# Optimization experiments

Measured on AMD Instinct MI355X. Metric: run time of the kernel, lower is better.

## Reference

```python
import jax, jax.numpy as jnp
import numpy as np

B, M, FIN, FOUT, K, E = 4, 50000, 128, 128, 4, 800000


def setup_inputs() -> dict:
    key = jax.random.key(0)
    ks = jax.random.split(key, 8)
    x = jax.random.normal(ks[0], (B, M, FIN), dtype=jnp.float32)
    L_rows = jax.random.randint(ks[1], (E,), 0, M, dtype=jnp.int32)
    L_cols = jax.random.randint(ks[2], (E,), 0, M, dtype=jnp.int32)
    # stands in for the rescaled (0.75 * (2L/lmax - I)) Laplacian values
    L_vals = jax.random.normal(ks[3], (E,), dtype=jnp.float32) * 0.05
    stddev = 1.0 / np.sqrt(FIN * (K + 0.5) / 2.0)
    kernel = jax.random.normal(ks[4], (K * FIN, FOUT), dtype=jnp.float32) * stddev
    W_down = jax.random.normal(ks[5], (FOUT, FOUT // 8), dtype=jnp.float32) * (1.0 / np.sqrt(FOUT))
    b_down = jnp.zeros((FOUT // 8,), dtype=jnp.float32)
    W_up = jax.random.normal(ks[6], (FOUT // 8, FOUT), dtype=jnp.float32) * (1.0 / np.sqrt(FOUT // 8))
    b_up = jnp.zeros((FOUT,), dtype=jnp.float32)
    return {"x": x, "L_vals": L_vals, "L_rows": L_rows, "L_cols": L_cols,
            "kernel": kernel, "W_down": W_down, "b_down": b_down,
            "W_up": W_up, "b_up": b_up}


def reference(x, L_vals, L_rows, L_cols, kernel, W_down, b_down, W_up, b_up):
    B_, M_, Fin = x.shape
    K_ = kernel.shape[0] // Fin

    def spmm(X):  # sparse L [M,M] @ dense X [M, D]
        return jax.ops.segment_sum(L_vals[:, None] * X[L_cols], L_rows, num_segments=M_)

    # Chebyshev recurrence, operating on [M, Fin*B] like the TF code
    x0 = x.transpose(1, 2, 0).reshape(M_, Fin * B_)
    stack = [x0]
    if K_ > 1:
        x1 = spmm(x0)
        stack.append(x1)
    for _ in range(2, K_):
        x2 = 2.0 * spmm(x1) - x0
        stack.append(x2)
        x0, x1 = x1, x2

    # [K,M,Fin*B] -> [K,M,Fin,B] -> [B,M,Fin,K] -> [B*M, Fin*K]
    xs = jnp.stack(stack, axis=0).reshape(K_, M_, Fin, B_)
    xs = xs.transpose(3, 1, 2, 0).reshape(B_ * M_, Fin * K_)
    y = (xs @ kernel).reshape(B_, M_, -1)
    y = jax.nn.relu(y)

    # SE block: avg-pool over nodes, down (swish), up (sigmoid), scale
    s = jnp.mean(y, axis=1, keepdims=True)          # [B, 1, Fout]
    d = jax.nn.swish(s @ W_down + b_down)           # [B, 1, Fout/8]
    u = jax.nn.sigmoid(d @ W_up + b_up)             # [B, 1, Fout]
    return y * u
```

## Files before the change

### kernel.cpp

```cpp
#include <hip/hip_runtime.h>
#include <hip/hip_bf16.h>

#define BB 4
#define MM 50000
#define FINF 128
#define FOUTF 128
#define KCH 4
#define EE 800000
#define NROWS (BB*MM)
#define XC 512
#define CD 512
#define SLABS 4
#define SC (XC/SLABS)
#define SCB 512
#define NSB ((MM + SCB - 1)/SCB)
#define GXB ((MM + 255)/256)

__device__ __forceinline__ float bf2f(unsigned short u){
    union{unsigned int i; float f;} v; v.i = ((unsigned int)u) << 16; return v.f;
}
__device__ __forceinline__ unsigned short f2bf(float f){
    union{float f; unsigned int i;} v; v.f = f;
    unsigned int r = v.i + 0x7FFF + ((v.i >> 16) & 1);
    return (unsigned short)(r >> 16);
}

typedef __bf16 bf16x8 __attribute__((ext_vector_type(8)));
typedef float  f32x4  __attribute__((ext_vector_type(4)));

typedef __attribute__((address_space(3))) unsigned int       lds_uint;
typedef const __attribute__((address_space(1))) unsigned int gbl_uint;

__global__ __launch_bounds__(256) void k_init_x0(const float* __restrict__ x,
                                                 unsigned short* __restrict__ X0){
    int tid = blockIdx.x*256 + threadIdx.x;
    if (tid >= BB*MM*FINF/4) return;
    int f4 = tid & 31;
    int t  = tid >> 5;
    int m  = t % MM, b = t / MM;
    float4 v = ((const float4*)x)[tid];
    ushort4 o;
    o.x = f2bf(v.x); o.y = f2bf(v.y); o.z = f2bf(v.z); o.w = f2bf(v.w);
    *(ushort4*)(X0 + (size_t)m*XC + b*FINF + f4*4) = o;
}

__global__ __launch_bounds__(256) void k_prepw(const float* __restrict__ kern,
                                               unsigned short* __restrict__ Wt){
    int tid = blockIdx.x*256 + threadIdx.x;
    int c = tid & 511, n = tid >> 9;
    int kc = c >> 7, f = c & 127;
    int ns = n >> 4, l16 = n & 15;
    int ks = c >> 5, rem = c & 31, g = rem >> 3, j = rem & 7;
    int lane = g*16 + l16;
    Wt[((ns*16 + ks)*64 + lane)*8 + j] = f2bf(kern[(f*KCH + kc)*FOUTF + n]);
}

__global__ __launch_bounds__(256) void k_hist(const int* __restrict__ rows, int* __restrict__ counts){
    int e = blockIdx.x*256 + threadIdx.x;
    if (e < EE) atomicAdd(&counts[rows[e]], 1);
}

__global__ __launch_bounds__(256) void k_scanA(const int* __restrict__ counts, int* __restrict__ part){
    __shared__ int red[256];
    int b = blockIdx.x, t = threadIdx.x;
    int i = b*SCB + t;
    int s = 0;
    if (i < MM) s += counts[i];
    if (i + 256 < (b+1)*SCB && i + 256 < MM) s += counts[i+256];
    red[t] = s; __syncthreads();
    for (int d = 128; d > 0; d >>= 1){
        if (t < d) red[t] += red[t+d];
        __syncthreads();
    }
    if (t == 0) part[b] = red[0];
}

__global__ __launch_bounds__(128) void k_scanB(int* __restrict__ part){
    __shared__ int sh[128];
    int t = threadIdx.x;
    sh[t] = (t < NSB) ? part[t] : 0;
    __syncthreads();
    for (int d = 1; d < 128; d <<= 1){
        int v = (t >= d) ? sh[t-d] : 0;
        __syncthreads();
        sh[t] += v;
        __syncthreads();
    }
    if (t < NSB) part[t] = sh[t];
}

__global__ __launch_bounds__(256) void k_scanC(const int* __restrict__ counts, const int* __restrict__ part,
                                               int* __restrict__ offs, int* __restrict__ cursor){
    __shared__ int sh[256];
    int b = blockIdx.x, t = threadIdx.x;
    int base = (b == 0) ? 0 : part[b-1];
    int i0 = b*SCB + 2*t;
    int c0 = (i0     < MM) ? counts[i0]   : 0;
    int c1 = (i0 + 1 < MM) ? counts[i0+1] : 0;
    sh[t] = c0 + c1; __syncthreads();
    for (int d = 1; d < 256; d <<= 1){
        int v = (t >= d) ? sh[t-d] : 0;
        __syncthreads();
        sh[t] += v;
        __syncthreads();
    }
    int excl = base + sh[t] - (c0 + c1);
    if (i0 < MM){ offs[i0] = excl;      cursor[i0] = excl; }
    if (i0 + 1 < MM){ offs[i0+1] = excl + c0; cursor[i0+1] = excl + c0; }
    if (b == gridDim.x-1 && t == 255) offs[MM] = EE;
}

__global__ __launch_bounds__(256) void k_scatter(const int* __restrict__ rows, const int* __restrict__ cols,
                                                 const float* __restrict__ vals, int* __restrict__ cursor,
                                                 int2* __restrict__ edges){
    int e = blockIdx.x*256 + threadIdx.x;
    if (e >= EE) return;
    int r = rows[e];
    int pos = atomicAdd(&cursor[r], 1);
    edges[pos] = make_int2(cols[e], __float_as_int(vals[e]));
}

__global__ __launch_bounds__(256) void k_spmm_slab(const unsigned short* __restrict__ Xin,
                                                   const unsigned short* __restrict__ Xprev,
                                                   unsigned short* __restrict__ Xout,
                                                   const int* __restrict__ offs,
                                                   const int2* __restrict__ edges,
                                                   float alpha, int sub, int cbase){
    int m    = blockIdx.x*4 + (threadIdx.x >> 6);
    int lane = threadIdx.x & 63;
    size_t c0 = (size_t)cbase + lane*2;
    int start = offs[m], end = offs[m+1];
    float a0 = 0.f, a1 = 0.f;

    int nb = (end - start) & ~3;
    int burst_end = start + nb;
    int j = start;

    int2 ee[4];
    if (j < burst_end){
        #pragma unroll
        for (int q = 0; q < 4; ++q) ee[q] = edges[j+q];
    }
    while (j < burst_end){
        int2 e_[4];
        #pragma unroll
        for (int q = 0; q < 4; ++q) e_[q] = ee[q];
        j += 4;
        if (j < burst_end){
            #pragma unroll
            for (int q = 0; q < 4; ++q) ee[q] = edges[j+q];
        }
        ushort2 xv[4];
        #pragma unroll
        for (int q = 0; q < 4; ++q)
            xv[q] = *(const ushort2*)(Xin + (size_t)e_[q].x*XC + c0);
        #pragma unroll
        for (int q = 0; q < 4; ++q){
            float val = __int_as_float(e_[q].y);
            a0 += val*bf2f(xv[q].x); a1 += val*bf2f(xv[q].y);
        }
    }
    for (; j < end; ++j){
        int2 e = edges[j];
        float val = __int_as_float(e.y);
        ushort2 xv = *(const ushort2*)(Xin + (size_t)e.x*XC + c0);
        a0 += val*bf2f(xv.x); a1 += val*bf2f(xv.y);
    }

    a0 *= alpha; a1 *= alpha;
    if (sub){
        ushort2 pv = *(const ushort2*)(Xprev + (size_t)m*XC + c0);
        a0 -= bf2f(pv.x); a1 -= bf2f(pv.y);
    }
    ushort2 o; o.x = f2bf(a0); o.y = f2bf(a1);
    *(ushort2*)(Xout + (size_t)m*XC + c0) = o;
}

__global__ __launch_bounds__(256, 2) void k_gemm(const unsigned short* __restrict__ X0,
                                                 const unsigned short* __restrict__ X1,
                                                 const unsigned short* __restrict__ X2,
                                                 const unsigned short* __restrict__ X3,
                                                 const unsigned short* __restrict__ Wt,
                                                 float* __restrict__ Y,
                                                 float* __restrict__ Ypart){
    const int wave = threadIdx.x >> 6;
    const int lane = threadIdx.x & 63;
    const int l16  = lane & 15;
    const int g    = lane >> 4;
    const int bidx = blockIdx.y;
    const int m0   = blockIdx.x*256;

    __shared__ unsigned short As[2][8192];
    __shared__ unsigned short Bs[2][4096];

    const unsigned short* const Xs[4] = {X0, X1, X2, X3};

    f32x4 acc[4][8];
    #pragma unroll
    for (int i = 0; i < 4; ++i)
        #pragma unroll
        for (int j = 0; j < 8; ++j) acc[i][j] = (f32x4){0.f,0.f,0.f,0.f};

    auto stage = [&](int buf, int ks){
        const unsigned short* Xb = Xs[ks >> 2];
        const int f0 = (ks & 3)*64;
        #pragma unroll
        for (int q = 0; q < 4; ++q){
            int row = q*64 + wave*16 + (lane >> 2);
            int mr  = m0 + row; if (mr >= MM) mr = MM-1;
            int inner = ((lane & 3)*16) ^ ((row & 6) << 3);
            const char* src = (const char*)Xb + (size_t)mr*1024 + bidx*256 + f0 + inner;
            lds_uint* dst = (lds_uint*)(&As[buf][(q*4096 + wave*1024)/2]);
            __builtin_amdgcn_global_load_lds((gbl_uint*)src, dst, 16, 0, 0);
        }
        #pragma unroll
        for (int q = 0; q < 2; ++q){
            int ns = q*4 + wave;
            const char* src = (const char*)Wt + (size_t)(ns*16 + ks)*1024 + lane*16;
            lds_uint* dst = (lds_uint*)(&Bs[buf][ns*512]);
            __builtin_amdgcn_global_load_lds((gbl_uint*)src, dst, 16, 0, 0);
        }
    };

    stage(0, 0);
    __syncthreads();

    for (int ks = 0; ks < 16; ++ks){
        const int buf = ks & 1;
        if (ks < 15) stage(buf ^ 1, ks + 1);

        bf16x8 a[4];
        #pragma unroll
        for (int i = 0; i < 4; ++i){
            int rr = wave*64 + i*16 + l16;
            int phys = rr*64 + ((g*16) ^ ((rr & 6) << 3));
            a[i] = *(const bf16x8*)((const char*)&As[buf][0] + phys);
        }
        #pragma unroll
        for (int ns = 0; ns < 8; ++ns){
            bf16x8 b = *(const bf16x8*)(&Bs[buf][ns*512 + lane*8]);
            #pragma unroll
            for (int i = 0; i < 4; ++i)
                acc[i][ns] = __builtin_amdgcn_mfma_f32_16x16x32_bf16(a[i], b, acc[i][ns], 0, 0, 0);
        }
        __syncthreads();
    }

    __shared__ float ldsum[4][FOUTF];
    float csum[8];
    #pragma unroll
    for (int ns = 0; ns < 8; ++ns) csum[ns] = 0.f;

    #pragma unroll
    for (int i = 0; i < 4; ++i){
        #pragma unroll
        for (int reg = 0; reg < 4; ++reg){
            int mr = m0 + wave*64 + i*16 + g*4 + reg;
            if (mr < MM){
                #pragma unroll
                for (int ns = 0; ns < 8; ++ns){
                    float v = acc[i][ns][reg];
                    v = v > 0.f ? v : 0.f;
                    Y[((size_t)bidx*MM + mr)*FOUTF + ns*16 + l16] = v;
                    csum[ns] += v;
                }
            }
        }
    }
    #pragma unroll
    for (int ns = 0; ns < 8; ++ns){
        float v = csum[ns];
        v += __shfl_xor(v, 16);
        v += __shfl_xor(v, 32);
        csum[ns] = v;
    }
    if (lane < 16){
        #pragma unroll
        for (int ns = 0; ns < 8; ++ns) ldsum[wave][ns*16 + lane] = csum[ns];
    }
    __syncthreads();
    int t = threadIdx.x;
    if (t < FOUTF){
        float s = ldsum[0][t] + ldsum[1][t] + ldsum[2][t] + ldsum[3][t];
        Ypart[((size_t)bidx*GXB + blockIdx.x)*FOUTF + t] = s;
    }
}

__global__ __launch_bounds__(128) void k_se(const float* __restrict__ Ypart,
                                            const float* __restrict__ Wd, const float* __restrict__ bd,
                                            const float* __restrict__ Wu, const float* __restrict__ bu,
                                            float* __restrict__ u){
    int b = blockIdx.x, t = threadIdx.x;
    __shared__ float sm[128];
    __shared__ float dsh[16];
    float s = 0.f;
    for (int j = 0; j < GXB; ++j) s += Ypart[((size_t)b*GXB + j)*FOUTF + t];
    sm[t] = s * (1.0f/MM);
    __syncthreads();
    if (t < 16){
        float a = bd[t];
        for (int f = 0; f < 128; ++f) a += sm[f]*Wd[f*16 + t];
        dsh[t] = a / (1.f + expf(-a));
    }
    __syncthreads();
    float a = bu[t];
    for (int j = 0; j < 16; ++j) a += dsh[j]*Wu[j*FOUTF + t];
    u[b*FOUTF + t] = 1.f/(1.f + expf(-a));
}

__global__ __launch_bounds__(256) void k_scale(const float* __restrict__ Y, const float* __restrict__ u,
                                               float* __restrict__ out){
    int tid = blockIdx.x*256 + threadIdx.x;
    if (tid >= NROWS*FOUTF/4) return;
    int b  = tid / (MM*FOUTF/4);
    int f4 = tid & 31;
    float4 yv = ((const float4*)Y)[tid];
    float4 uv = *(const float4*)(u + b*FOUTF + f4*4);
    float4 o;
    o.x = yv.x*uv.x; o.y = yv.y*uv.y; o.z = yv.z*uv.z; o.w = yv.w*uv.w;
    ((float4*)out)[tid] = o;
}

extern "C" void kernel_launch(void* const* d_in, const int* in_sizes, int n_in,
                              void* d_out, int out_size, void* d_ws, size_t ws_size,
                              hipStream_t stream){
    (void)in_sizes; (void)n_in; (void)out_size; (void)ws_size;
    const float* x    = (const float*)d_in[0];
    const float* lv   = (const float*)d_in[1];
    const int*   lr   = (const int*)d_in[2];
    const int*   lc   = (const int*)d_in[3];
    const float* kern = (const float*)d_in[4];
    const float* Wd   = (const float*)d_in[5];
    const float* bd   = (const float*)d_in[6];
    const float* Wu   = (const float*)d_in[7];
    const float* bu   = (const float*)d_in[8];
    float* out = (float*)d_out;

    char* w = (char*)d_ws;
    size_t off = 0;
    auto take = [&](size_t bytes)->char*{
        char* p = w + off; off += (bytes + 255) & ~(size_t)255; return p;
    };
    unsigned short* X[4];
    for (int i = 0; i < 4; ++i) X[i] = (unsigned short*)take((size_t)MM*XC*2);
    float* Y           = (float*)take((size_t)NROWS*FOUTF*4);
    unsigned short* Wt = (unsigned short*)take((size_t)FOUTF*CD*2);
    int* counts        = (int*)take((size_t)MM*4);
    int* offs          = (int*)take((size_t)(MM+1)*4);
    int* cursor        = (int*)take((size_t)MM*4);
    int2* edges        = (int2*)take((size_t)EE*8);
    int* part          = (int*)take((size_t)NSB*4);
    float* Ypart       = (float*)take((size_t)BB*GXB*FOUTF*4);
    float* u           = (float*)take((size_t)BB*FOUTF*4);

    hipMemsetAsync(counts, 0, MM*4, stream);

    k_init_x0<<<25000, 256, 0, stream>>>(x, X[0]);
    k_prepw<<<256, 256, 0, stream>>>(kern, Wt);
    k_hist<<<(EE+255)/256, 256, 0, stream>>>(lr, counts);
    k_scanA<<<NSB, 256, 0, stream>>>(counts, part);
    k_scanB<<<1, 128, 0, stream>>>(part);
    k_scanC<<<NSB, 256, 0, stream>>>(counts, part, offs, cursor);
    k_scatter<<<(EE+255)/256, 256, 0, stream>>>(lr, lc, lv, cursor, edges);

    for (int s = 0; s < SLABS; ++s){
        int cbase = s*SC;
        k_spmm_slab<<<MM/4, 256, 0, stream>>>(X[0], X[0], X[1], offs, edges, 1.0f, 0, cbase);
        k_spmm_slab<<<MM/4, 256, 0, stream>>>(X[1], X[0], X[2], offs, edges, 2.0f, 1, cbase);
        k_spmm_slab<<<MM/4, 256, 0, stream>>>(X[2], X[1], X[3], offs, edges, 2.0f, 1, cbase);
    }

    dim3 ggemm(GXB, BB);
    k_gemm<<<ggemm, 256, 0, stream>>>(X[0], X[1], X[2], X[3], Wt, Y, Ypart);

    k_se<<<BB, 128, 0, stream>>>(Ypart, Wd, bd, Wu, bu, u);
    k_scale<<<25000, 256, 0, stream>>>(Y, u, out);
}
```

Baseline: 790.9 us.

## Replace slab SpMM with XCD-aware column-strip SpMM splitting edges across lane groups

Replaces the four-slab loop of SpMM launches with a single launch per Chebyshev step. Each block id is decoded so that each of the 8 XCDs handles a fixed 64-column strip (16 strips over two halves), which keeps each XCD's L2 working set to its own columns. Within a wave, four 16-lane groups process different edges in parallel, each lane loading 4 bytes, and the partial sums are reduced with shuffles. Edge column indices are pre-shifted to byte offsets in the scatter kernel to save address arithmetic. The cost is extra shuffle reductions, masked tail loads, and reliance on the hardware assigning consecutive blocks round-robin across XCDs.

```diff
diff --git a/kernel.cpp b/kernel.cpp
--- a/kernel.cpp
+++ b/kernel.cpp
@@ -10,11 +10,12 @@
 #define NROWS (BB*MM)
 #define XC 512
 #define CD 512
-#define SLABS 4
-#define SC (XC/SLABS)
 #define SCB 512
 #define NSB ((MM + SCB - 1)/SCB)
 #define GXB ((MM + 255)/256)
+#define NSS 16
+#define RPB 16
+#define RBS (MM/RPB)
 
 __device__ __forceinline__ float bf2f(unsigned short u){
     union{unsigned int i; float f;} v; v.i = ((unsigned int)u) << 16; return v.f;
@@ -117,63 +118,59 @@
     if (e >= EE) return;
     int r = rows[e];
     int pos = atomicAdd(&cursor[r], 1);
-    edges[pos] = make_int2(cols[e], __float_as_int(vals[e]));
-}
-
-__global__ __launch_bounds__(256) void k_spmm_slab(const unsigned short* __restrict__ Xin,
-                                                   const unsigned short* __restrict__ Xprev,
-                                                   unsigned short* __restrict__ Xout,
-                                                   const int* __restrict__ offs,
-                                                   const int2* __restrict__ edges,
-                                                   float alpha, int sub, int cbase){
-    int m    = blockIdx.x*4 + (threadIdx.x >> 6);
-    int lane = threadIdx.x & 63;
-    size_t c0 = (size_t)cbase + lane*2;
-    int start = offs[m], end = offs[m+1];
+    edges[pos] = make_int2(cols[e] << 10, __float_as_int(vals[e]));
+}
+
+__global__ __launch_bounds__(1024) void k_spmm_x(const unsigned short* __restrict__ Xin,
+                                                 const unsigned short* __restrict__ Xprev,
+                                                 unsigned short* __restrict__ Xout,
+                                                 const int* __restrict__ offs,
+                                                 const int2* __restrict__ edges,
+                                                 float alpha, int sub){
+    const int i    = blockIdx.x;
+    const int xcd  = i & 7;
+    const int j2   = i >> 3;
+    const int half = (j2 >= RBS) ? 1 : 0;
+    const int ss   = xcd + (half << 3);
+    const int rb   = j2 - half*RBS;
+    const int wave = threadIdx.x >> 6;
+    const int m    = rb*RPB + wave;
+    const int lane = threadIdx.x & 63;
+    const int qg   = lane >> 4;
+    const int cl   = lane & 15;
+    const int cb   = ss*64 + cl*4;
+
+    const int start = offs[m], end = offs[m+1];
     float a0 = 0.f, a1 = 0.f;
-
-    int nb = (end - start) & ~3;
-    int burst_end = start + nb;
-    int j = start;
-
-    int2 ee[4];
-    if (j < burst_end){
-        #pragma unroll
-        for (int q = 0; q < 4; ++q) ee[q] = edges[j+q];
-    }
-    while (j < burst_end){
-        int2 e_[4];
-        #pragma unroll
-        for (int q = 0; q < 4; ++q) e_[q] = ee[q];
-        j += 4;
-        if (j < burst_end){
-            #pragma unroll
-            for (int q = 0; q < 4; ++q) ee[q] = edges[j+q];
-        }
-        ushort2 xv[4];
-        #pragma unroll
-        for (int q = 0; q < 4; ++q)
-            xv[q] = *(const ushort2*)(Xin + (size_t)e_[q].x*XC + c0);
-        #pragma unroll
-        for (int q = 0; q < 4; ++q){
-            float val = __int_as_float(e_[q].y);
-            a0 += val*bf2f(xv[q].x); a1 += val*bf2f(xv[q].y);
-        }
-    }
-    for (; j < end; ++j){
-        int2 e = edges[j];
-        float val = __int_as_float(e.y);
-        ushort2 xv = *(const ushort2*)(Xin + (size_t)e.x*XC + c0);
-        a0 += val*bf2f(xv.x); a1 += val*bf2f(xv.y);
-    }
-
+    const char* __restrict__ bp = (const char*)Xin;
+    const long long* __restrict__ ep = (const long long*)edges;
+    for (int j = start; j < end; j += 8){
+        #pragma unroll
+        for (int q = 0; q < 2; ++q){
+            int je = j + q*4 + qg;
+            bool ok = je < end;
+            long long ev = __builtin_nontemporal_load(ep + (ok ? je : 0));
+            float val = ok ? __int_as_float((int)(ev >> 32)) : 0.f;
+            unsigned int xv = *(const unsigned int*)(bp + (unsigned)(int)ev + cb);
+            union{unsigned int u; float f;} lo, hi;
+            lo.u = xv << 16; hi.u = xv & 0xffff0000u;
+            a0 += val*lo.f; a1 += val*hi.f;
+        }
+    }
+    a0 += __shfl_xor(a0, 16); a0 += __shfl_xor(a0, 32);
+    a1 += __shfl_xor(a1, 16); a1 += __shfl_xor(a1, 32);
     a0 *= alpha; a1 *= alpha;
+    size_t ob = (size_t)m*1024 + cb;
     if (sub){
-        ushort2 pv = *(const ushort2*)(Xprev + (size_t)m*XC + c0);
-        a0 -= bf2f(pv.x); a1 -= bf2f(pv.y);
-    }
-    ushort2 o; o.x = f2bf(a0); o.y = f2bf(a1);
-    *(ushort2*)(Xout + (size_t)m*XC + c0) = o;
+        unsigned int pv = *(const unsigned int*)((const char*)Xprev + ob);
+        union{unsigned int u; float f;} lo, hi;
+        lo.u = pv << 16; hi.u = pv & 0xffff0000u;
+        a0 -= lo.f; a1 -= hi.f;
+    }
+    if (qg == 0){
+        unsigned int o = ((unsigned int)f2bf(a1) << 16) | (unsigned int)f2bf(a0);
+        *(unsigned int*)((char*)Xout + ob) = o;
+    }
 }
 
 __global__ __launch_bounds__(256, 2) void k_gemm(const unsigned short* __restrict__ X0,
@@ -363,12 +360,9 @@
     k_scanC<<<NSB, 256, 0, stream>>>(counts, part, offs, cursor);
     k_scatter<<<(EE+255)/256, 256, 0, stream>>>(lr, lc, lv, cursor, edges);
 
-    for (int s = 0; s < SLABS; ++s){
-        int cbase = s*SC;
-        k_spmm_slab<<<MM/4, 256, 0, stream>>>(X[0], X[0], X[1], offs, edges, 1.0f, 0, cbase);
-        k_spmm_slab<<<MM/4, 256, 0, stream>>>(X[1], X[0], X[2], offs, edges, 2.0f, 1, cbase);
-        k_spmm_slab<<<MM/4, 256, 0, stream>>>(X[2], X[1], X[3], offs, edges, 2.0f, 1, cbase);
-    }
+    k_spmm_x<<<NSS*RBS, 1024, 0, stream>>>(X[0], X[0], X[1], offs, edges, 1.0f, 0);
+    k_spmm_x<<<NSS*RBS, 1024, 0, stream>>>(X[1], X[0], X[2], offs, edges, 2.0f, 1);
+    k_spmm_x<<<NSS*RBS, 1024, 0, stream>>>(X[2], X[1], X[3], offs, edges, 2.0f, 1);
 
     dim3 ggemm(GXB, BB);
     k_gemm<<<ggemm, 256, 0, stream>>>(X[0], X[1], X[2], X[3], Wt, Y, Ypart);
```

After: 1.666 ms. +110.6%, slower.

## Replace slabbed SpMM with full-width 16-byte-per-lane SpMM and fuse scan

Applied to the files above, without the earlier changes.

The SpMM is no longer split into four 128-column slabs (12 launches). Each wave now processes a full 512-column bf16 row, with each lane loading 16 bytes per edge and edges walked once per Chebyshev step. Column indices are pre-shifted into byte offsets during scatter, and tail edges are padded by masking instead of a scalar remainder loop. The separate scanB kernel is removed: each scanC block sums the preceding partials itself, which costs a little redundant work and drops one launch. Wider per-lane loads raise register use and give up the L2 locality the slabbing provided for the gathered rows.

```diff
diff --git a/kernel.cpp b/kernel.cpp
--- a/kernel.cpp
+++ b/kernel.cpp
@@ -10,8 +10,6 @@
 #define NROWS (BB*MM)
 #define XC 512
 #define CD 512
-#define SLABS 4
-#define SC (XC/SLABS)
 #define SCB 512
 #define NSB ((MM + SCB - 1)/SCB)
 #define GXB ((MM + 255)/256)
@@ -75,29 +73,18 @@
     if (t == 0) part[b] = red[0];
 }
 
-__global__ __launch_bounds__(128) void k_scanB(int* __restrict__ part){
-    __shared__ int sh[128];
-    int t = threadIdx.x;
-    sh[t] = (t < NSB) ? part[t] : 0;
-    __syncthreads();
-    for (int d = 1; d < 128; d <<= 1){
-        int v = (t >= d) ? sh[t-d] : 0;
-        __syncthreads();
-        sh[t] += v;
-        __syncthreads();
-    }
-    if (t < NSB) part[t] = sh[t];
-}
-
 __global__ __launch_bounds__(256) void k_scanC(const int* __restrict__ counts, const int* __restrict__ part,
                                                int* __restrict__ offs, int* __restrict__ cursor){
     __shared__ int sh[256];
+    __shared__ int pp[NSB];
     int b = blockIdx.x, t = threadIdx.x;
-    int base = (b == 0) ? 0 : part[b-1];
+    if (t < NSB) pp[t] = part[t];
     int i0 = b*SCB + 2*t;
     int c0 = (i0     < MM) ? counts[i0]   : 0;
     int c1 = (i0 + 1 < MM) ? counts[i0+1] : 0;
     sh[t] = c0 + c1; __syncthreads();
+    int base = 0;
+    for (int i = 0; i < b; ++i) base += pp[i];
     for (int d = 1; d < 256; d <<= 1){
         int v = (t >= d) ? sh[t-d] : 0;
         __syncthreads();
@@ -117,63 +104,96 @@
     if (e >= EE) return;
     int r = rows[e];
     int pos = atomicAdd(&cursor[r], 1);
-    edges[pos] = make_int2(cols[e], __float_as_int(vals[e]));
-}
-
-__global__ __launch_bounds__(256) void k_spmm_slab(const unsigned short* __restrict__ Xin,
-                                                   const unsigned short* __restrict__ Xprev,
-                                                   unsigned short* __restrict__ Xout,
-                                                   const int* __restrict__ offs,
-                                                   const int2* __restrict__ edges,
-                                                   float alpha, int sub, int cbase){
-    int m    = blockIdx.x*4 + (threadIdx.x >> 6);
-    int lane = threadIdx.x & 63;
-    size_t c0 = (size_t)cbase + lane*2;
-    int start = offs[m], end = offs[m+1];
-    float a0 = 0.f, a1 = 0.f;
-
-    int nb = (end - start) & ~3;
-    int burst_end = start + nb;
-    int j = start;
-
-    int2 ee[4];
-    if (j < burst_end){
-        #pragma unroll
-        for (int q = 0; q < 4; ++q) ee[q] = edges[j+q];
-    }
-    while (j < burst_end){
-        int2 e_[4];
-        #pragma unroll
-        for (int q = 0; q < 4; ++q) e_[q] = ee[q];
-        j += 4;
-        if (j < burst_end){
-            #pragma unroll
-            for (int q = 0; q < 4; ++q) ee[q] = edges[j+q];
-        }
-        ushort2 xv[4];
-        #pragma unroll
-        for (int q = 0; q < 4; ++q)
-            xv[q] = *(const ushort2*)(Xin + (size_t)e_[q].x*XC + c0);
-        #pragma unroll
-        for (int q = 0; q < 4; ++q){
-            float val = __int_as_float(e_[q].y);
-            a0 += val*bf2f(xv[q].x); a1 += val*bf2f(xv[q].y);
-        }
-    }
-    for (; j < end; ++j){
-        int2 e = edges[j];
-        float val = __int_as_float(e.y);
-        ushort2 xv = *(const ushort2*)(Xin + (size_t)e.x*XC + c0);
-        a0 += val*bf2f(xv.x); a1 += val*bf2f(xv.y);
-    }
-
-    a0 *= alpha; a1 *= alpha;
+    edges[pos] = make_int2(cols[e] << 10, __float_as_int(vals[e]));
+}
+
+__global__ __launch_bounds__(256) void k_spmm_w(const unsigned short* __restrict__ Xin,
+                                                const unsigned short* __restrict__ Xprev,
+                                                unsigned short* __restrict__ Xout,
+                                                const int* __restrict__ offs,
+                                                const int2* __restrict__ edges,
+                                                float alpha, int sub){
+    const int m    = blockIdx.x*4 + (threadIdx.x >> 6);
+    const int lane = threadIdx.x & 63;
+    const int cb   = lane*16;
+    const int start = offs[m], end = offs[m+1];
+
+    float acc[8];
+    #pragma unroll
+    for (int d = 0; d < 8; ++d) acc[d] = 0.f;
+
+    const char* __restrict__ bp = (const char*)Xin;
+    const long long* __restrict__ ep = (const long long*)edges;
+
+    if (start < end){
+        const long long base = ep[start];
+        const int basec = (int)base;
+        int  c[4]; float v[4];
+        {
+            #pragma unroll
+            for (int q = 0; q < 4; ++q){
+                int je = start + q;
+                bool ok = je < end;
+                long long e = ok ? ep[je] : base;
+                c[q] = ok ? (int)e : basec;
+                v[q] = ok ? __int_as_float((int)(e >> 32)) : 0.f;
+            }
+        }
+        int j = start;
+        while (j < end){
+            int cc[4]; float vv[4];
+            #pragma unroll
+            for (int q = 0; q < 4; ++q){ cc[q] = c[q]; vv[q] = v[q]; }
+            j += 4;
+            if (j < end){
+                #pragma unroll
+                for (int q = 0; q < 4; ++q){
+                    int je = j + q;
+                    bool ok = je < end;
+                    long long e = ok ? ep[je] : base;
+                    c[q] = ok ? (int)e : basec;
+                    v[q] = ok ? __int_as_float((int)(e >> 32)) : 0.f;
+                }
+            }
+            uint4 x[4];
+            #pragma unroll
+            for (int q = 0; q < 4; ++q)
+                x[q] = *(const uint4*)(bp + (unsigned)cc[q] + cb);
+            #pragma unroll
+            for (int q = 0; q < 4; ++q){
+                const unsigned int* xw = (const unsigned int*)&x[q];
+                #pragma unroll
+                for (int d = 0; d < 4; ++d){
+                    unsigned int u = xw[d];
+                    union{unsigned int ui; float f;} lo, hi;
+                    lo.ui = u << 16; hi.ui = u & 0xffff0000u;
+                    acc[d*2]   += vv[q]*lo.f;
+                    acc[d*2+1] += vv[q]*hi.f;
+                }
+            }
+        }
+    }
+
+    #pragma unroll
+    for (int d = 0; d < 8; ++d) acc[d] *= alpha;
+    size_t ob = (size_t)m*1024 + cb;
     if (sub){
-        ushort2 pv = *(const ushort2*)(Xprev + (size_t)m*XC + c0);
-        a0 -= bf2f(pv.x); a1 -= bf2f(pv.y);
-    }
-    ushort2 o; o.x = f2bf(a0); o.y = f2bf(a1);
-    *(ushort2*)(Xout + (size_t)m*XC + c0) = o;
+        uint4 pv = *(const uint4*)((const char*)Xprev + ob);
+        const unsigned int* pw = (const unsigned int*)&pv;
+        #pragma unroll
+        for (int d = 0; d < 4; ++d){
+            unsigned int u = pw[d];
+            union{unsigned int ui; float f;} lo, hi;
+            lo.ui = u << 16; hi.ui = u & 0xffff0000u;
+            acc[d*2]   -= lo.f;
+            acc[d*2+1] -= hi.f;
+        }
+    }
+    unsigned int o[4];
+    #pragma unroll
+    for (int d = 0; d < 4; ++d)
+        o[d] = ((unsigned int)f2bf(acc[d*2+1]) << 16) | (unsigned int)f2bf(acc[d*2]);
+    *(uint4*)((char*)Xout + ob) = *(const uint4*)o;
 }
 
 __global__ __launch_bounds__(256, 2) void k_gemm(const unsigned short* __restrict__ X0,
@@ -359,16 +379,12 @@
     k_prepw<<<256, 256, 0, stream>>>(kern, Wt);
     k_hist<<<(EE+255)/256, 256, 0, stream>>>(lr, counts);
     k_scanA<<<NSB, 256, 0, stream>>>(counts, part);
-    k_scanB<<<1, 128, 0, stream>>>(part);
     k_scanC<<<NSB, 256, 0, stream>>>(counts, part, offs, cursor);
     k_scatter<<<(EE+255)/256, 256, 0, stream>>>(lr, lc, lv, cursor, edges);
 
-    for (int s = 0; s < SLABS; ++s){
-        int cbase = s*SC;
-        k_spmm_slab<<<MM/4, 256, 0, stream>>>(X[0], X[0], X[1], offs, edges, 1.0f, 0, cbase);
-        k_spmm_slab<<<MM/4, 256, 0, stream>>>(X[1], X[0], X[2], offs, edges, 2.0f, 1, cbase);
-        k_spmm_slab<<<MM/4, 256, 0, stream>>>(X[2], X[1], X[3], offs, edges, 2.0f, 1, cbase);
-    }
+    k_spmm_w<<<MM/4, 256, 0, stream>>>(X[0], X[0], X[1], offs, edges, 1.0f, 0);
+    k_spmm_w<<<MM/4, 256, 0, stream>>>(X[1], X[0], X[2], offs, edges, 2.0f, 1);
+    k_spmm_w<<<MM/4, 256, 0, stream>>>(X[2], X[1], X[3], offs, edges, 2.0f, 1);
 
     dim3 ggemm(GXB, BB);
     k_gemm<<<ggemm, 256, 0, stream>>>(X[0], X[1], X[2], X[3], Wt, Y, Ypart);
```

After: 748.7 us. 1.06x faster.
